# Kernel optimization log

Measured on AMD Instinct MI355X. Metric: run time of the kernel, lower is better.

The kernel has to match this reference:

```python
import jax, jax.numpy as jnp
import numpy as np

B, S, H, I, E, K = 2, 512, 1024, 4096, 8, 2
LN_EPS = 1e-5


def setup_inputs() -> dict:
    key = jax.random.key(0)
    ks = jax.random.split(key, 5)
    sc = 0.02  # init scale for weights
    return {
        "hidden_states": jax.random.normal(ks[0], (B, S, H), jnp.float32),
        "ln_w": jnp.ones((H,), jnp.float32),
        "ln_b": jnp.zeros((H,), jnp.float32),
        "Wr": jax.random.normal(ks[1], (E, H), jnp.float32) * sc,  # router [out=E, in=H]
        "br": jnp.zeros((E,), jnp.float32),
        "W1": jax.random.normal(ks[2], (E, I, H), jnp.float32) * sc,  # dense1 per expert [out=I, in=H]
        "b1": jnp.zeros((E, I), jnp.float32),
        "W2": jax.random.normal(ks[3], (E, H, I), jnp.float32) * sc,  # dense2 per expert [out=H, in=I]
        "b2": jnp.zeros((E, H), jnp.float32),
    }


def reference(hidden_states, ln_w, ln_b, Wr, br, W1, b1, W2, b2):
    # Eval mode: no jitter noise, no dropout.
    residual = hidden_states
    mu = jnp.mean(hidden_states, axis=-1, keepdims=True)
    var = jnp.mean(jnp.square(hidden_states - mu), axis=-1, keepdims=True)
    x = (hidden_states - mu) * jax.lax.rsqrt(var + LN_EPS) * ln_w + ln_b  # [B,S,H]

    logits = jnp.einsum("bsh,eh->bse", x, Wr) + br  # [B,S,E]
    topw, topi = jax.lax.top_k(logits, K)  # [B,S,K]
    topw = jax.nn.softmax(topw, axis=-1)
    # Combine weights per expert (top-k indices are distinct, so scatter == first-match)
    combine = jnp.sum(jax.nn.one_hot(topi, E, dtype=x.dtype) * topw[..., None], axis=-2)  # [B,S,E]

    # Dense per-expert FFN (reference form of gather-FFN-scatter); combine zeros out unselected experts
    a = jax.nn.gelu(jnp.einsum("bsh,eih->bsei", x, W1) + b1, approximate=False)  # [B,S,E,I]
    y = jnp.einsum("bsei,ehi->bseh", a, W2) + b2  # [B,S,E,H]
    out = residual + jnp.einsum("bse,bseh->bsh", combine, y)

    probs = jax.nn.softmax(logits, axis=-1)
    usage = jnp.mean(probs, axis=(0, 1))  # [E]
    balance_loss = E * jnp.sum(usage * usage) - 1.0
    return out, balance_loss
```

## Files before the change

### kernel.cpp

```cpp
#include <hip/hip_runtime.h>
#include <hip/hip_bf16.h>
#include <math.h>
#include <stdint.h>

#define T_TOK 1024
#define H_DIM 1024
#define I_DIM 4096
#define E_NUM 8
#define NSLOT (2 * T_TOK)

typedef __attribute__((ext_vector_type(8))) short bf16x8;
typedef __attribute__((ext_vector_type(4))) float f32x4;

#define MFMA_BF16(a, b, c) __builtin_amdgcn_mfma_f32_16x16x32_bf16(a, b, c, 0, 0, 0)

__device__ __forceinline__ short f2bf(float f) {
  union { float f; unsigned u; } x; x.f = f;
  unsigned r = (x.u + 0x7fffu + ((x.u >> 16) & 1u)) >> 16;
  return (short)r;
}
__device__ __forceinline__ int pack2bf(float a, float b) {
  return ((int)(unsigned short)f2bf(a)) | (((int)f2bf(b)) << 16);
}

typedef __attribute__((address_space(3))) unsigned int as3_u32;
typedef const __attribute__((address_space(1))) unsigned int as1_u32c;
__device__ __forceinline__ void glds16(const void* g, void* l) {
  __builtin_amdgcn_global_load_lds((as1_u32c*)g, (as3_u32*)l, 16, 0, 0);
}

__global__ __launch_bounds__(256) void k_ln_router(
    const float* __restrict__ x, const float* __restrict__ ln_w,
    const float* __restrict__ ln_b, const float* __restrict__ Wr,
    const float* __restrict__ br,
    short* __restrict__ xln, int* __restrict__ sel_e, float* __restrict__ sel_w,
    float* __restrict__ probs) {
  const int t = blockIdx.x;
  const int tid = threadIdx.x;
  const int lane = tid & 63, wid = tid >> 6;
  __shared__ float sx[H_DIM];
  __shared__ float redS[8];
  __shared__ float slog[E_NUM];

  float4 v = ((const float4*)(x + (size_t)t * H_DIM))[tid];
  float s = v.x + v.y + v.z + v.w;
  float ss = v.x * v.x + v.y * v.y + v.z * v.z + v.w * v.w;
  for (int o = 32; o > 0; o >>= 1) { s += __shfl_down(s, o); ss += __shfl_down(ss, o); }
  if (lane == 0) { redS[wid] = s; redS[4 + wid] = ss; }
  __syncthreads();
  float st = redS[0] + redS[1] + redS[2] + redS[3];
  float sst = redS[4] + redS[5] + redS[6] + redS[7];
  float mu = st * (1.0f / H_DIM);
  float var = sst * (1.0f / H_DIM) - mu * mu;
  float rs = rsqrtf(var + 1e-5f);

  float4 lw = ((const float4*)ln_w)[tid];
  float4 lb = ((const float4*)ln_b)[tid];
  float4 xn;
  xn.x = (v.x - mu) * rs * lw.x + lb.x;
  xn.y = (v.y - mu) * rs * lw.y + lb.y;
  xn.z = (v.z - mu) * rs * lw.z + lb.z;
  xn.w = (v.w - mu) * rs * lw.w + lb.w;
  sx[4 * tid + 0] = xn.x; sx[4 * tid + 1] = xn.y;
  sx[4 * tid + 2] = xn.z; sx[4 * tid + 3] = xn.w;
  short4 s4;
  s4.x = f2bf(xn.x); s4.y = f2bf(xn.y); s4.z = f2bf(xn.z); s4.w = f2bf(xn.w);
  ((short4*)(xln + (size_t)t * H_DIM))[tid] = s4;
  __syncthreads();

  for (int e = 2 * wid; e < 2 * wid + 2; ++e) {
    float p = 0.f;
    for (int h = lane; h < H_DIM; h += 64) p += sx[h] * Wr[e * H_DIM + h];
    for (int o = 32; o > 0; o >>= 1) p += __shfl_down(p, o);
    if (lane == 0) slog[e] = p + br[e];
  }
  __syncthreads();

  if (tid == 0) {
    float lg[E_NUM];
    for (int e = 0; e < E_NUM; ++e) lg[e] = slog[e];
    int i0 = 0;
    for (int e = 1; e < E_NUM; ++e) if (lg[e] > lg[i0]) i0 = e;
    int i1 = (i0 == 0) ? 1 : 0;
    for (int e = 0; e < E_NUM; ++e) if (e != i0 && lg[e] > lg[i1]) i1 = e;
    float w1e = __expf(lg[i1] - lg[i0]);
    float den = 1.f + w1e;
    sel_e[2 * t] = i0; sel_w[2 * t] = 1.f / den;
    sel_e[2 * t + 1] = i1; sel_w[2 * t + 1] = w1e / den;
    float se = 0.f, pe[E_NUM];
    for (int e = 0; e < E_NUM; ++e) { pe[e] = __expf(lg[e] - lg[i0]); se += pe[e]; }
    float inv = 1.f / se;
    for (int e = 0; e < E_NUM; ++e) probs[t * E_NUM + e] = pe[e] * inv;
  }
}

__global__ __launch_bounds__(512) void k_route(
    const int* __restrict__ sel_e, const float* __restrict__ probs,
    int* __restrict__ counts, int* __restrict__ basep,
    int* __restrict__ tlist, int* __restrict__ sel_idx,
    float* __restrict__ loss_out) {
  const int wid = threadIdx.x >> 6;
  const int lane = threadIdx.x & 63;
  __shared__ int scnt[E_NUM];
  __shared__ float susage[E_NUM];

  int cnt = 0;
  for (int s0 = 0; s0 < NSLOT; s0 += 64) {
    int s = s0 + lane;
    bool m = (sel_e[s] == wid);
    unsigned long long mk = __ballot(m);
    int pre = __popcll(mk & ((1ULL << lane) - 1ULL));
    if (m) {
      int idx = cnt + pre;
      sel_idx[s] = idx;
      tlist[wid * T_TOK + idx] = s >> 1;
    }
    cnt += __popcll(mk);
  }
  if (lane == 0) scnt[wid] = cnt;

  float u = 0.f;
  for (int t = lane; t < T_TOK; t += 64) u += probs[t * E_NUM + wid];
  for (int o = 32; o > 0; o >>= 1) u += __shfl_down(u, o);
  if (lane == 0) susage[wid] = u * (1.0f / T_TOK);
  __syncthreads();

  if (threadIdx.x == 0) {
    int b = 0;
    for (int e = 0; e < E_NUM; ++e) { basep[e] = b; counts[e] = scnt[e]; b += scnt[e]; }
    float sq = 0.f;
    for (int e = 0; e < E_NUM; ++e) sq += susage[e] * susage[e];
    *loss_out = (float)E_NUM * sq - 1.0f;
  }
}

__global__ __launch_bounds__(256) void k_ffn1(
    const short* __restrict__ xln, const float* __restrict__ W1,
    const float* __restrict__ b1, const int* __restrict__ counts,
    const int* __restrict__ basep, const int* __restrict__ tlist,
    short* __restrict__ a_buf) {
  const int e = blockIdx.z;
  const int cnt = counts[e];
  const int m0 = blockIdx.y * 128;
  if (m0 >= cnt) return;
  const int n0 = blockIdx.x * 128;

  __shared__ __align__(16) short As[128 * 32];
  __shared__ __align__(16) short Bs[128][40];

  const int tid = threadIdx.x;
  const int lane = tid & 63;
  const int wid = tid >> 6;
  const int wr = wid >> 1, wc = wid & 1;
  const int fr = lane & 15, fq = lane >> 4;

  const int arow = tid >> 2;
  const int au = (tid & 3) * 8;
  int r0 = m0 + arow;       if (r0 >= cnt) r0 = cnt - 1;
  int r1 = m0 + 64 + arow;  if (r1 >= cnt) r1 = cnt - 1;
  const short* ag0 = xln + (size_t)tlist[e * T_TOK + r0] * H_DIM + au;
  const short* ag1 = xln + (size_t)tlist[e * T_TOK + r1] * H_DIM + au;
  short* al0 = As + (size_t)tid * 8;
  short* al1 = As + (size_t)(256 + tid) * 8;

  const int bcol = (tid & 7) * 4;
  const int brow = tid >> 3;
  const float* bg = W1 + ((size_t)e * I_DIM + n0 + brow) * H_DIM + bcol;
  float4 breg[4];

#define LOADB(kk)                                                        \
  {                                                                      \
    _Pragma("unroll") for (int i = 0; i < 4; ++i)                        \
        breg[i] = *(const float4*)(bg + (size_t)(i * 32) * H_DIM + (kk));\
  }
#define CVTW()                                                           \
  {                                                                      \
    _Pragma("unroll") for (int i = 0; i < 4; ++i) {                      \
      int2 p;                                                            \
      p.x = pack2bf(breg[i].x, breg[i].y);                               \
      p.y = pack2bf(breg[i].z, breg[i].w);                               \
      *(int2*)&Bs[brow + i * 32][bcol] = p;                              \
    }                                                                    \
  }
#define GLDS(kk)                                                         \
  { glds16(ag0 + (kk), al0); glds16(ag1 + (kk), al1); }

  f32x4 acc[4][4];
#pragma unroll
  for (int i = 0; i < 4; ++i)
#pragma unroll
    for (int j = 0; j < 4; ++j) acc[i][j] = (f32x4)0.f;

  LOADB(0);
  GLDS(0);
  CVTW();
  __syncthreads();

  for (int kt = 0; kt < H_DIM / 32; ++kt) {
    const int kn = (kt + 1) * 32;
    const bool last = (kt == H_DIM / 32 - 1);
    if (!last) LOADB(kn);
    bf16x8 af[4], bb[4];
#pragma unroll
    for (int mi = 0; mi < 4; ++mi)
      af[mi] = *(const bf16x8*)(As + (wr * 64 + mi * 16 + fr) * 32 + fq * 8);
#pragma unroll
    for (int ni = 0; ni < 4; ++ni)
      bb[ni] = *(const bf16x8*)&Bs[wc * 64 + ni * 16 + fr][fq * 8];
#pragma unroll
    for (int mi = 0; mi < 4; ++mi)
#pragma unroll
      for (int ni = 0; ni < 4; ++ni)
        acc[mi][ni] = MFMA_BF16(af[mi], bb[ni], acc[mi][ni]);
    __syncthreads();
    if (!last) {
      GLDS(kn);
      CVTW();
      __syncthreads();
    }
  }

  const int slot0 = basep[e] + m0;
  float b1v[4];
#pragma unroll
  for (int ni = 0; ni < 4; ++ni)
    b1v[ni] = b1[e * I_DIM + n0 + wc * 64 + ni * 16 + fr];
#pragma unroll
  for (int mi = 0; mi < 4; ++mi)
#pragma unroll
    for (int j = 0; j < 4; ++j) {
      int r = wr * 64 + mi * 16 + fq * 4 + j;
      if (m0 + r < cnt) {
        size_t rowoff = (size_t)(slot0 + r) * I_DIM;
#pragma unroll
        for (int ni = 0; ni < 4; ++ni) {
          int colg = n0 + wc * 64 + ni * 16 + fr;
          float vv = acc[mi][ni][j] + b1v[ni];
          float g = 0.5f * vv * (1.0f + erff(vv * 0.70710678118654752f));
          a_buf[rowoff + colg] = f2bf(g);
        }
      }
    }
#undef LOADB
#undef CVTW
#undef GLDS
}

__global__ __launch_bounds__(256) void k_ffn2(
    const short* __restrict__ a_buf, const float* __restrict__ W2,
    const int* __restrict__ counts, const int* __restrict__ basep,
    float* __restrict__ y_part, int lg) {
  const int z = blockIdx.z;
  const int e = z >> lg;
  const int kc = z & ((1 << lg) - 1);
  const int CH = I_DIM >> lg;
  const int cnt = counts[e];
  const int m0 = blockIdx.y * 128;
  if (m0 >= cnt) return;
  const int n0 = blockIdx.x * 128;

  __shared__ __align__(16) short As[128 * 32];
  __shared__ __align__(16) short Bs[128][40];

  const int tid = threadIdx.x;
  const int lane = tid & 63;
  const int wid = tid >> 6;
  const int wr = wid >> 1, wc = wid & 1;
  const int fr = lane & 15, fq = lane >> 4;

  const int arow = tid >> 2;
  const int au = (tid & 3) * 8;
  int r0 = m0 + arow;       if (r0 >= cnt) r0 = cnt - 1;
  int r1 = m0 + 64 + arow;  if (r1 >= cnt) r1 = cnt - 1;
  const int sb = basep[e];
  const short* ag0 = a_buf + (size_t)(sb + r0) * I_DIM + kc * CH + au;
  const short* ag1 = a_buf + (size_t)(sb + r1) * I_DIM + kc * CH + au;
  short* al0 = As + (size_t)tid * 8;
  short* al1 = As + (size_t)(256 + tid) * 8;

  const int bcol = (tid & 7) * 4;
  const int brow = tid >> 3;
  const float* bg = W2 + ((size_t)e * H_DIM + n0 + brow) * I_DIM + kc * CH + bcol;
  float4 breg[4];

#define LOADB(kk)                                                        \
  {                                                                      \
    _Pragma("unroll") for (int i = 0; i < 4; ++i)                        \
        breg[i] = *(const float4*)(bg + (size_t)(i * 32) * I_DIM + (kk));\
  }
#define CVTW()                                                           \
  {                                                                      \
    _Pragma("unroll") for (int i = 0; i < 4; ++i) {                      \
      int2 p;                                                            \
      p.x = pack2bf(breg[i].x, breg[i].y);                               \
      p.y = pack2bf(breg[i].z, breg[i].w);                               \
      *(int2*)&Bs[brow + i * 32][bcol] = p;                              \
    }                                                                    \
  }
#define GLDS(kk)                                                         \
  { glds16(ag0 + (kk), al0); glds16(ag1 + (kk), al1); }

  f32x4 acc[4][4];
#pragma unroll
  for (int i = 0; i < 4; ++i)
#pragma unroll
    for (int j = 0; j < 4; ++j) acc[i][j] = (f32x4)0.f;

  LOADB(0);
  GLDS(0);
  CVTW();
  __syncthreads();

  const int KT = CH / 32;
  for (int kt = 0; kt < KT; ++kt) {
    const int kn = (kt + 1) * 32;
    const bool last = (kt == KT - 1);
    if (!last) LOADB(kn);
    bf16x8 af[4], bb[4];
#pragma unroll
    for (int mi = 0; mi < 4; ++mi)
      af[mi] = *(const bf16x8*)(As + (wr * 64 + mi * 16 + fr) * 32 + fq * 8);
#pragma unroll
    for (int ni = 0; ni < 4; ++ni)
      bb[ni] = *(const bf16x8*)&Bs[wc * 64 + ni * 16 + fr][fq * 8];
#pragma unroll
    for (int mi = 0; mi < 4; ++mi)
#pragma unroll
      for (int ni = 0; ni < 4; ++ni)
        acc[mi][ni] = MFMA_BF16(af[mi], bb[ni], acc[mi][ni]);
    __syncthreads();
    if (!last) {
      GLDS(kn);
      CVTW();
      __syncthreads();
    }
  }

  const int slot0 = sb + m0;
  float* yp = y_part + (size_t)kc * ((size_t)NSLOT * H_DIM);
#pragma unroll
  for (int mi = 0; mi < 4; ++mi)
#pragma unroll
    for (int j = 0; j < 4; ++j) {
      int r = wr * 64 + mi * 16 + fq * 4 + j;
      if (m0 + r < cnt) {
        size_t rowoff = (size_t)(slot0 + r) * H_DIM;
#pragma unroll
        for (int ni = 0; ni < 4; ++ni) {
          int colg = n0 + wc * 64 + ni * 16 + fr;
          yp[rowoff + colg] = acc[mi][ni][j];
        }
      }
    }
#undef LOADB
#undef CVTW
#undef GLDS
}

__global__ __launch_bounds__(256) void k_combine(
    const float* __restrict__ hidden, const float* __restrict__ y_part,
    const float* __restrict__ b2, const int* __restrict__ basep,
    const int* __restrict__ sel_e, const int* __restrict__ sel_idx,
    const float* __restrict__ sel_w, float* __restrict__ out, int KS) {
  const int t = blockIdx.x;
  const int tid = threadIdx.x;
  int e0 = sel_e[2 * t], e1 = sel_e[2 * t + 1];
  int s0 = basep[e0] + sel_idx[2 * t];
  int s1 = basep[e1] + sel_idx[2 * t + 1];
  float w0 = sel_w[2 * t], w1 = sel_w[2 * t + 1];
  const size_t TY = (size_t)NSLOT * H_DIM;
  float4 y0 = make_float4(0.f, 0.f, 0.f, 0.f);
  float4 y1 = make_float4(0.f, 0.f, 0.f, 0.f);
  for (int kc = 0; kc < KS; ++kc) {
    float4 p0 = ((const float4*)(y_part + kc * TY + (size_t)s0 * H_DIM))[tid];
    float4 p1 = ((const float4*)(y_part + kc * TY + (size_t)s1 * H_DIM))[tid];
    y0.x += p0.x; y0.y += p0.y; y0.z += p0.z; y0.w += p0.w;
    y1.x += p1.x; y1.y += p1.y; y1.z += p1.z; y1.w += p1.w;
  }
  float4 be0 = ((const float4*)(b2 + (size_t)e0 * H_DIM))[tid];
  float4 be1 = ((const float4*)(b2 + (size_t)e1 * H_DIM))[tid];
  float4 r = ((const float4*)(hidden + (size_t)t * H_DIM))[tid];
  float4 o;
  o.x = r.x + w0 * (y0.x + be0.x) + w1 * (y1.x + be1.x);
  o.y = r.y + w0 * (y0.y + be0.y) + w1 * (y1.y + be1.y);
  o.z = r.z + w0 * (y0.z + be0.z) + w1 * (y1.z + be1.z);
  o.w = r.w + w0 * (y0.w + be0.w) + w1 * (y1.w + be1.w);
  ((float4*)(out + (size_t)t * H_DIM))[tid] = o;
}

extern "C" void kernel_launch(void* const* d_in, const int* in_sizes, int n_in,
                              void* d_out, int out_size, void* d_ws, size_t ws_size,
                              hipStream_t stream) {
  const float* hidden = (const float*)d_in[0];
  const float* ln_w = (const float*)d_in[1];
  const float* ln_b = (const float*)d_in[2];
  const float* Wr = (const float*)d_in[3];
  const float* br = (const float*)d_in[4];
  const float* W1 = (const float*)d_in[5];
  const float* b1 = (const float*)d_in[6];
  const float* W2 = (const float*)d_in[7];
  const float* b2 = (const float*)d_in[8];
  float* out = (float*)d_out;

  char* w = (char*)d_ws;
  int* counts = (int*)(w + 0);
  int* basep = (int*)(w + 256);
  float* probs = (float*)(w + 512);
  int* tlist = (int*)(w + 33280);
  int* sel_e = (int*)(w + 66048);
  int* sel_idx = (int*)(w + 74240);
  float* sel_w = (float*)(w + 82432);
  short* xln = (short*)(w + 98304);
  short* a_buf = (short*)(w + 98304 + 2097152);
  const size_t Y_OFF = 98304 + 2097152 + 16777216;
  float* y_part = (float*)(w + Y_OFF);
  const size_t Y_SZ = (size_t)NSLOT * H_DIM * 4;
  int lg = 2;
  while (lg > 0 && Y_OFF + (Y_SZ << lg) > ws_size) --lg;
  const int KS = 1 << lg;

  k_ln_router<<<T_TOK, 256, 0, stream>>>(hidden, ln_w, ln_b, Wr, br, xln,
                                         sel_e, sel_w, probs);
  k_route<<<1, 512, 0, stream>>>(sel_e, probs, counts, basep, tlist, sel_idx,
                                 out + (size_t)T_TOK * H_DIM);
  k_ffn1<<<dim3(I_DIM / 128, T_TOK / 128, E_NUM), 256, 0, stream>>>(
      xln, W1, b1, counts, basep, tlist, a_buf);
  k_ffn2<<<dim3(H_DIM / 128, T_TOK / 128, E_NUM << lg), 256, 0, stream>>>(
      a_buf, W2, counts, basep, y_part, lg);
  k_combine<<<T_TOK, 256, 0, stream>>>(hidden, y_part, b2, basep, sel_e, sel_idx,
                                       sel_w, out, KS);
}
```

Before: 200.2 us.

## Double-buffer LDS in expert GEMMs and shrink N tile to 64

```diff
diff --git a/kernel.cpp b/kernel.cpp
--- a/kernel.cpp
+++ b/kernel.cpp
@@ -143,88 +143,78 @@
   const int cnt = counts[e];
   const int m0 = blockIdx.y * 128;
   if (m0 >= cnt) return;
-  const int n0 = blockIdx.x * 128;
-
-  __shared__ __align__(16) short As[128 * 32];
-  __shared__ __align__(16) short Bs[128][40];
+  const int n0 = blockIdx.x * 64;
+
+  __shared__ __align__(16) short As[2][4096];
+  __shared__ __align__(16) short Bs[2][64][40];
 
   const int tid = threadIdx.x;
-  const int lane = tid & 63;
-  const int wid = tid >> 6;
+  const int lane = tid & 63, wid = tid >> 6;
   const int wr = wid >> 1, wc = wid & 1;
   const int fr = lane & 15, fq = lane >> 4;
 
-  const int arow = tid >> 2;
-  const int au = (tid & 3) * 8;
-  int r0 = m0 + arow;       if (r0 >= cnt) r0 = cnt - 1;
-  int r1 = m0 + 64 + arow;  if (r1 >= cnt) r1 = cnt - 1;
-  const short* ag0 = xln + (size_t)tlist[e * T_TOK + r0] * H_DIM + au;
-  const short* ag1 = xln + (size_t)tlist[e * T_TOK + r1] * H_DIM + au;
-  short* al0 = As + (size_t)tid * 8;
-  short* al1 = As + (size_t)(256 + tid) * 8;
-
-  const int bcol = (tid & 7) * 4;
-  const int brow = tid >> 3;
-  const float* bg = W1 + ((size_t)e * I_DIM + n0 + brow) * H_DIM + bcol;
-  float4 breg[4];
-
-#define LOADB(kk)                                                        \
-  {                                                                      \
-    _Pragma("unroll") for (int i = 0; i < 4; ++i)                        \
-        breg[i] = *(const float4*)(bg + (size_t)(i * 32) * H_DIM + (kk));\
-  }
-#define CVTW()                                                           \
-  {                                                                      \
-    _Pragma("unroll") for (int i = 0; i < 4; ++i) {                      \
-      int2 p;                                                            \
-      p.x = pack2bf(breg[i].x, breg[i].y);                               \
-      p.y = pack2bf(breg[i].z, breg[i].w);                               \
-      *(int2*)&Bs[brow + i * 32][bcol] = p;                              \
-    }                                                                    \
-  }
-#define GLDS(kk)                                                         \
-  { glds16(ag0 + (kk), al0); glds16(ag1 + (kk), al1); }
-
-  f32x4 acc[4][4];
-#pragma unroll
-  for (int i = 0; i < 4; ++i)
-#pragma unroll
-    for (int j = 0; j < 4; ++j) acc[i][j] = (f32x4)0.f;
-
-  LOADB(0);
-  GLDS(0);
-  CVTW();
-  __syncthreads();
-
+  const int arow = tid & 127;
+  const int afq = tid >> 7;
+  int rA = m0 + arow; if (rA >= cnt) rA = cnt - 1;
+  const short* ag = xln + (size_t)tlist[e * T_TOK + rA] * H_DIM + afq * 8;
+
+  const int brow = tid >> 2, bseg = (tid & 3) * 8;
+  const float* bg = W1 + ((size_t)e * I_DIM + n0 + brow) * H_DIM + bseg;
+
+  f32x4 acc[4][2];
+#pragma unroll
+  for (int i = 0; i < 4; ++i) { acc[i][0] = (f32x4)0.f; acc[i][1] = (f32x4)0.f; }
+
+  float4 b0 = *(const float4*)(bg);
+  float4 b1r = *(const float4*)(bg + 4);
+  glds16(ag, &As[0][(size_t)tid * 8]);
+  glds16(ag + 16, &As[0][(size_t)(256 + tid) * 8]);
+  {
+    int4 p;
+    p.x = pack2bf(b0.x, b0.y); p.y = pack2bf(b0.z, b0.w);
+    p.z = pack2bf(b1r.x, b1r.y); p.w = pack2bf(b1r.z, b1r.w);
+    *(int4*)&Bs[0][brow][bseg] = p;
+  }
+  __syncthreads();
+
+  int cur = 0;
   for (int kt = 0; kt < H_DIM / 32; ++kt) {
     const int kn = (kt + 1) * 32;
-    const bool last = (kt == H_DIM / 32 - 1);
-    if (!last) LOADB(kn);
-    bf16x8 af[4], bb[4];
+    const bool pf = (kt + 1 < H_DIM / 32);
+    float4 nb0, nb1;
+    if (pf) {
+      glds16(ag + kn, &As[cur ^ 1][(size_t)tid * 8]);
+      glds16(ag + kn + 16, &As[cur ^ 1][(size_t)(256 + tid) * 8]);
+      nb0 = *(const float4*)(bg + kn);
+      nb1 = *(const float4*)(bg + kn + 4);
+    }
+    bf16x8 af[4], bb[2];
 #pragma unroll
     for (int mi = 0; mi < 4; ++mi)
-      af[mi] = *(const bf16x8*)(As + (wr * 64 + mi * 16 + fr) * 32 + fq * 8);
-#pragma unroll
-    for (int ni = 0; ni < 4; ++ni)
-      bb[ni] = *(const bf16x8*)&Bs[wc * 64 + ni * 16 + fr][fq * 8];
+      af[mi] = *(const bf16x8*)&As[cur][(fq * 128 + wr * 64 + mi * 16 + fr) * 8];
+#pragma unroll
+    for (int ni = 0; ni < 2; ++ni)
+      bb[ni] = *(const bf16x8*)&Bs[cur][wc * 32 + ni * 16 + fr][fq * 8];
 #pragma unroll
     for (int mi = 0; mi < 4; ++mi)
 #pragma unroll
-      for (int ni = 0; ni < 4; ++ni)
+      for (int ni = 0; ni < 2; ++ni)
         acc[mi][ni] = MFMA_BF16(af[mi], bb[ni], acc[mi][ni]);
+    if (pf) {
+      int4 p;
+      p.x = pack2bf(nb0.x, nb0.y); p.y = pack2bf(nb0.z, nb0.w);
+      p.z = pack2bf(nb1.x, nb1.y); p.w = pack2bf(nb1.z, nb1.w);
+      *(int4*)&Bs[cur ^ 1][brow][bseg] = p;
+    }
     __syncthreads();
-    if (!last) {
-      GLDS(kn);
-      CVTW();
-      __syncthreads();
-    }
+    cur ^= 1;
   }
 
   const int slot0 = basep[e] + m0;
-  float b1v[4];
-#pragma unroll
-  for (int ni = 0; ni < 4; ++ni)
-    b1v[ni] = b1[e * I_DIM + n0 + wc * 64 + ni * 16 + fr];
+  float b1v[2];
+#pragma unroll
+  for (int ni = 0; ni < 2; ++ni)
+    b1v[ni] = b1[e * I_DIM + n0 + wc * 32 + ni * 16 + fr];
 #pragma unroll
   for (int mi = 0; mi < 4; ++mi)
 #pragma unroll
@@ -233,17 +223,14 @@
       if (m0 + r < cnt) {
         size_t rowoff = (size_t)(slot0 + r) * I_DIM;
 #pragma unroll
-        for (int ni = 0; ni < 4; ++ni) {
-          int colg = n0 + wc * 64 + ni * 16 + fr;
+        for (int ni = 0; ni < 2; ++ni) {
+          int colg = n0 + wc * 32 + ni * 16 + fr;
           float vv = acc[mi][ni][j] + b1v[ni];
           float g = 0.5f * vv * (1.0f + erff(vv * 0.70710678118654752f));
           a_buf[rowoff + colg] = f2bf(g);
         }
       }
     }
-#undef LOADB
-#undef CVTW
-#undef GLDS
 }
 
 __global__ __launch_bounds__(256) void k_ffn2(
@@ -257,83 +244,73 @@
   const int cnt = counts[e];
   const int m0 = blockIdx.y * 128;
   if (m0 >= cnt) return;
-  const int n0 = blockIdx.x * 128;
-
-  __shared__ __align__(16) short As[128 * 32];
-  __shared__ __align__(16) short Bs[128][40];
+  const int n0 = blockIdx.x * 64;
+
+  __shared__ __align__(16) short As[2][4096];
+  __shared__ __align__(16) short Bs[2][64][40];
 
   const int tid = threadIdx.x;
-  const int lane = tid & 63;
-  const int wid = tid >> 6;
+  const int lane = tid & 63, wid = tid >> 6;
   const int wr = wid >> 1, wc = wid & 1;
   const int fr = lane & 15, fq = lane >> 4;
 
-  const int arow = tid >> 2;
-  const int au = (tid & 3) * 8;
-  int r0 = m0 + arow;       if (r0 >= cnt) r0 = cnt - 1;
-  int r1 = m0 + 64 + arow;  if (r1 >= cnt) r1 = cnt - 1;
+  const int arow = tid & 127;
+  const int afq = tid >> 7;
+  int rA = m0 + arow; if (rA >= cnt) rA = cnt - 1;
   const int sb = basep[e];
-  const short* ag0 = a_buf + (size_t)(sb + r0) * I_DIM + kc * CH + au;
-  const short* ag1 = a_buf + (size_t)(sb + r1) * I_DIM + kc * CH + au;
-  short* al0 = As + (size_t)tid * 8;
-  short* al1 = As + (size_t)(256 + tid) * 8;
-
-  const int bcol = (tid & 7) * 4;
-  const int brow = tid >> 3;
-  const float* bg = W2 + ((size_t)e * H_DIM + n0 + brow) * I_DIM + kc * CH + bcol;
-  float4 breg[4];
-
-#define LOADB(kk)                                                        \
-  {                                                                      \
-    _Pragma("unroll") for (int i = 0; i < 4; ++i)                        \
-        breg[i] = *(const float4*)(bg + (size_t)(i * 32) * I_DIM + (kk));\
-  }
-#define CVTW()                                                           \
-  {                                                                      \
-    _Pragma("unroll") for (int i = 0; i < 4; ++i) {                      \
-      int2 p;                                                            \
-      p.x = pack2bf(breg[i].x, breg[i].y);                               \
-      p.y = pack2bf(breg[i].z, breg[i].w);                               \
-      *(int2*)&Bs[brow + i * 32][bcol] = p;                              \
-    }                                                                    \
-  }
-#define GLDS(kk)                                                         \
-  { glds16(ag0 + (kk), al0); glds16(ag1 + (kk), al1); }
-
-  f32x4 acc[4][4];
-#pragma unroll
-  for (int i = 0; i < 4; ++i)
-#pragma unroll
-    for (int j = 0; j < 4; ++j) acc[i][j] = (f32x4)0.f;
-
-  LOADB(0);
-  GLDS(0);
-  CVTW();
+  const short* ag = a_buf + (size_t)(sb + rA) * I_DIM + kc * CH + afq * 8;
+
+  const int brow = tid >> 2, bseg = (tid & 3) * 8;
+  const float* bg = W2 + ((size_t)e * H_DIM + n0 + brow) * I_DIM + kc * CH + bseg;
+
+  f32x4 acc[4][2];
+#pragma unroll
+  for (int i = 0; i < 4; ++i) { acc[i][0] = (f32x4)0.f; acc[i][1] = (f32x4)0.f; }
+
+  float4 b0 = *(const float4*)(bg);
+  float4 b1r = *(const float4*)(bg + 4);
+  glds16(ag, &As[0][(size_t)tid * 8]);
+  glds16(ag + 16, &As[0][(size_t)(256 + tid) * 8]);
+  {
+    int4 p;
+    p.x = pack2bf(b0.x, b0.y); p.y = pack2bf(b0.z, b0.w);
+    p.z = pack2bf(b1r.x, b1r.y); p.w = pack2bf(b1r.z, b1r.w);
+    *(int4*)&Bs[0][brow][bseg] = p;
+  }
   __syncthreads();
 
   const int KT = CH / 32;
+  int cur = 0;
   for (int kt = 0; kt < KT; ++kt) {
     const int kn = (kt + 1) * 32;
-    const bool last = (kt == KT - 1);
-    if (!last) LOADB(kn);
-    bf16x8 af[4], bb[4];
+    const bool pf = (kt + 1 < KT);
+    float4 nb0, nb1;
+    if (pf) {
+      glds16(ag + kn, &As[cur ^ 1][(size_t)tid * 8]);
+      glds16(ag + kn + 16, &As[cur ^ 1][(size_t)(256 + tid) * 8]);
+      nb0 = *(const float4*)(bg + kn);
+      nb1 = *(const float4*)(bg + kn + 4);
+    }
+    bf16x8 af[4], bb[2];
 #pragma unroll
     for (int mi = 0; mi < 4; ++mi)
-      af[mi] = *(const bf16x8*)(As + (wr * 64 + mi * 16 + fr) * 32 + fq * 8);
-#pragma unroll
-    for (int ni = 0; ni < 4; ++ni)
-      bb[ni] = *(const bf16x8*)&Bs[wc * 64 + ni * 16 + fr][fq * 8];
+      af[mi] = *(const bf16x8*)&As[cur][(fq * 128 + wr * 64 + mi * 16 + fr) * 8];
+#pragma unroll
+    for (int ni = 0; ni < 2; ++ni)
+      bb[ni] = *(const bf16x8*)&Bs[cur][wc * 32 + ni * 16 + fr][fq * 8];
 #pragma unroll
     for (int mi = 0; mi < 4; ++mi)
 #pragma unroll
-      for (int ni = 0; ni < 4; ++ni)
+      for (int ni = 0; ni < 2; ++ni)
         acc[mi][ni] = MFMA_BF16(af[mi], bb[ni], acc[mi][ni]);
+    if (pf) {
+      int4 p;
+      p.x = pack2bf(nb0.x, nb0.y); p.y = pack2bf(nb0.z, nb0.w);
+      p.z = pack2bf(nb1.x, nb1.y); p.w = pack2bf(nb1.z, nb1.w);
+      *(int4*)&Bs[cur ^ 1][brow][bseg] = p;
+    }
     __syncthreads();
-    if (!last) {
-      GLDS(kn);
-      CVTW();
-      __syncthreads();
-    }
+    cur ^= 1;
   }
 
   const int slot0 = sb + m0;
@@ -346,15 +323,12 @@
       if (m0 + r < cnt) {
         size_t rowoff = (size_t)(slot0 + r) * H_DIM;
 #pragma unroll
-        for (int ni = 0; ni < 4; ++ni) {
-          int colg = n0 + wc * 64 + ni * 16 + fr;
+        for (int ni = 0; ni < 2; ++ni) {
+          int colg = n0 + wc * 32 + ni * 16 + fr;
           yp[rowoff + colg] = acc[mi][ni][j];
         }
       }
     }
-#undef LOADB
-#undef CVTW
-#undef GLDS
 }
 
 __global__ __launch_bounds__(256) void k_combine(
@@ -423,9 +397,9 @@
                                          sel_e, sel_w, probs);
   k_route<<<1, 512, 0, stream>>>(sel_e, probs, counts, basep, tlist, sel_idx,
                                  out + (size_t)T_TOK * H_DIM);
-  k_ffn1<<<dim3(I_DIM / 128, T_TOK / 128, E_NUM), 256, 0, stream>>>(
+  k_ffn1<<<dim3(I_DIM / 64, T_TOK / 128, E_NUM), 256, 0, stream>>>(
       xln, W1, b1, counts, basep, tlist, a_buf);
-  k_ffn2<<<dim3(H_DIM / 128, T_TOK / 128, E_NUM << lg), 256, 0, stream>>>(
+  k_ffn2<<<dim3(H_DIM / 64, T_TOK / 128, E_NUM << lg), 256, 0, stream>>>(
       a_buf, W2, counts, basep, y_part, lg);
   k_combine<<<T_TOK, 256, 0, stream>>>(hidden, y_part, b2, basep, sel_e, sel_idx,
                                        sel_w, out, KS);
```

Result: slower. 254.2 us (+27.0%).

## Double-buffer FFN GEMMs with direct fp32 weight loads to swizzled LDS

Applied to the files above, without the earlier changes.

```diff
diff --git a/kernel.cpp b/kernel.cpp
--- a/kernel.cpp
+++ b/kernel.cpp
@@ -28,6 +28,8 @@
 __device__ __forceinline__ void glds16(const void* g, void* l) {
   __builtin_amdgcn_global_load_lds((as1_u32c*)g, (as3_u32*)l, 16, 0, 0);
 }
+
+union BBCast { int4 i4; bf16x8 v; };
 
 __global__ __launch_bounds__(256) void k_ln_router(
     const float* __restrict__ x, const float* __restrict__ ln_w,
@@ -145,45 +147,22 @@
   if (m0 >= cnt) return;
   const int n0 = blockIdx.x * 128;
 
-  __shared__ __align__(16) short As[128 * 32];
-  __shared__ __align__(16) short Bs[128][40];
+  __shared__ __align__(16) short As[2][128 * 32];
+  __shared__ __align__(16) float Bsf[2][128 * 32];
 
   const int tid = threadIdx.x;
-  const int lane = tid & 63;
-  const int wid = tid >> 6;
+  const int lane = tid & 63, wid = tid >> 6;
   const int wr = wid >> 1, wc = wid & 1;
   const int fr = lane & 15, fq = lane >> 4;
 
-  const int arow = tid >> 2;
-  const int au = (tid & 3) * 8;
-  int r0 = m0 + arow;       if (r0 >= cnt) r0 = cnt - 1;
-  int r1 = m0 + 64 + arow;  if (r1 >= cnt) r1 = cnt - 1;
-  const short* ag0 = xln + (size_t)tlist[e * T_TOK + r0] * H_DIM + au;
-  const short* ag1 = xln + (size_t)tlist[e * T_TOK + r1] * H_DIM + au;
-  short* al0 = As + (size_t)tid * 8;
-  short* al1 = As + (size_t)(256 + tid) * 8;
-
-  const int bcol = (tid & 7) * 4;
-  const int brow = tid >> 3;
-  const float* bg = W1 + ((size_t)e * I_DIM + n0 + brow) * H_DIM + bcol;
-  float4 breg[4];
-
-#define LOADB(kk)                                                        \
-  {                                                                      \
-    _Pragma("unroll") for (int i = 0; i < 4; ++i)                        \
-        breg[i] = *(const float4*)(bg + (size_t)(i * 32) * H_DIM + (kk));\
-  }
-#define CVTW()                                                           \
-  {                                                                      \
-    _Pragma("unroll") for (int i = 0; i < 4; ++i) {                      \
-      int2 p;                                                            \
-      p.x = pack2bf(breg[i].x, breg[i].y);                               \
-      p.y = pack2bf(breg[i].z, breg[i].w);                               \
-      *(int2*)&Bs[brow + i * 32][bcol] = p;                              \
-    }                                                                    \
-  }
-#define GLDS(kk)                                                         \
-  { glds16(ag0 + (kk), al0); glds16(ag1 + (kk), al1); }
+  int r0 = m0 + (tid >> 2); if (r0 >= cnt) r0 = cnt - 1;
+  int r1 = m0 + 64 + (tid >> 2); if (r1 >= cnt) r1 = cnt - 1;
+  const short* ag0 = xln + (size_t)tlist[e * T_TOK + r0] * H_DIM + (tid & 3) * 8;
+  const short* ag1 = xln + (size_t)tlist[e * T_TOK + r1] * H_DIM + (tid & 3) * 8;
+
+  const int bro = tid >> 3;
+  const int bslot = (tid & 7) ^ (bro & 7);
+  const float* bg = W1 + ((size_t)e * I_DIM + n0 + bro) * H_DIM + bslot * 4;
 
   f32x4 acc[4][4];
 #pragma unroll
@@ -191,33 +170,44 @@
 #pragma unroll
     for (int j = 0; j < 4; ++j) acc[i][j] = (f32x4)0.f;
 
-  LOADB(0);
-  GLDS(0);
-  CVTW();
-  __syncthreads();
-
+#define STAGE(kk, buf)                                                      \
+  {                                                                         \
+    glds16(ag0 + (kk), &As[buf][tid * 8]);                                  \
+    glds16(ag1 + (kk), &As[buf][(256 + tid) * 8]);                          \
+    _Pragma("unroll") for (int i = 0; i < 4; ++i)                           \
+        glds16(bg + (size_t)(i * 32) * H_DIM + (kk),                        \
+               &Bsf[buf][(i * 256 + tid) * 4]);                             \
+  }
+
+  STAGE(0, 0);
+  __syncthreads();
+
+  int cur = 0;
   for (int kt = 0; kt < H_DIM / 32; ++kt) {
-    const int kn = (kt + 1) * 32;
-    const bool last = (kt == H_DIM / 32 - 1);
-    if (!last) LOADB(kn);
+    if (kt + 1 < H_DIM / 32) STAGE((kt + 1) * 32, cur ^ 1);
     bf16x8 af[4], bb[4];
 #pragma unroll
     for (int mi = 0; mi < 4; ++mi)
-      af[mi] = *(const bf16x8*)(As + (wr * 64 + mi * 16 + fr) * 32 + fq * 8);
-#pragma unroll
-    for (int ni = 0; ni < 4; ++ni)
-      bb[ni] = *(const bf16x8*)&Bs[wc * 64 + ni * 16 + fr][fq * 8];
+      af[mi] = *(const bf16x8*)&As[cur][(wr * 64 + mi * 16 + fr) * 32 + fq * 8];
+#pragma unroll
+    for (int ni = 0; ni < 4; ++ni) {
+      const int row = wc * 64 + ni * 16 + fr;
+      const int base = row * 128 + fq * 32;
+      const int sw = (row & 7) << 4;
+      f32x4 lo = *(const f32x4*)((const char*)&Bsf[cur][0] + (base ^ sw));
+      f32x4 hi = *(const f32x4*)((const char*)&Bsf[cur][0] + ((base + 16) ^ sw));
+      BBCast c;
+      c.i4.x = pack2bf(lo[0], lo[1]); c.i4.y = pack2bf(lo[2], lo[3]);
+      c.i4.z = pack2bf(hi[0], hi[1]); c.i4.w = pack2bf(hi[2], hi[3]);
+      bb[ni] = c.v;
+    }
 #pragma unroll
     for (int mi = 0; mi < 4; ++mi)
 #pragma unroll
       for (int ni = 0; ni < 4; ++ni)
         acc[mi][ni] = MFMA_BF16(af[mi], bb[ni], acc[mi][ni]);
     __syncthreads();
-    if (!last) {
-      GLDS(kn);
-      CVTW();
-      __syncthreads();
-    }
+    cur ^= 1;
   }
 
   const int slot0 = basep[e] + m0;
@@ -241,9 +231,7 @@
         }
       }
     }
-#undef LOADB
-#undef CVTW
-#undef GLDS
+#undef STAGE
 }
 
 __global__ __launch_bounds__(256) void k_ffn2(
@@ -259,46 +247,23 @@
   if (m0 >= cnt) return;
   const int n0 = blockIdx.x * 128;
 
-  __shared__ __align__(16) short As[128 * 32];
-  __shared__ __align__(16) short Bs[128][40];
+  __shared__ __align__(16) short As[2][128 * 32];
+  __shared__ __align__(16) float Bsf[2][128 * 32];
 
   const int tid = threadIdx.x;
-  const int lane = tid & 63;
-  const int wid = tid >> 6;
+  const int lane = tid & 63, wid = tid >> 6;
   const int wr = wid >> 1, wc = wid & 1;
   const int fr = lane & 15, fq = lane >> 4;
 
-  const int arow = tid >> 2;
-  const int au = (tid & 3) * 8;
-  int r0 = m0 + arow;       if (r0 >= cnt) r0 = cnt - 1;
-  int r1 = m0 + 64 + arow;  if (r1 >= cnt) r1 = cnt - 1;
+  int r0 = m0 + (tid >> 2); if (r0 >= cnt) r0 = cnt - 1;
+  int r1 = m0 + 64 + (tid >> 2); if (r1 >= cnt) r1 = cnt - 1;
   const int sb = basep[e];
-  const short* ag0 = a_buf + (size_t)(sb + r0) * I_DIM + kc * CH + au;
-  const short* ag1 = a_buf + (size_t)(sb + r1) * I_DIM + kc * CH + au;
-  short* al0 = As + (size_t)tid * 8;
-  short* al1 = As + (size_t)(256 + tid) * 8;
-
-  const int bcol = (tid & 7) * 4;
-  const int brow = tid >> 3;
-  const float* bg = W2 + ((size_t)e * H_DIM + n0 + brow) * I_DIM + kc * CH + bcol;
-  float4 breg[4];
-
-#define LOADB(kk)                                                        \
-  {                                                                      \
-    _Pragma("unroll") for (int i = 0; i < 4; ++i)                        \
-        breg[i] = *(const float4*)(bg + (size_t)(i * 32) * I_DIM + (kk));\
-  }
-#define CVTW()                                                           \
-  {                                                                      \
-    _Pragma("unroll") for (int i = 0; i < 4; ++i) {                      \
-      int2 p;                                                            \
-      p.x = pack2bf(breg[i].x, breg[i].y);                               \
-      p.y = pack2bf(breg[i].z, breg[i].w);                               \
-      *(int2*)&Bs[brow + i * 32][bcol] = p;                              \
-    }                                                                    \
-  }
-#define GLDS(kk)                                                         \
-  { glds16(ag0 + (kk), al0); glds16(ag1 + (kk), al1); }
+  const short* ag0 = a_buf + (size_t)(sb + r0) * I_DIM + kc * CH + (tid & 3) * 8;
+  const short* ag1 = a_buf + (size_t)(sb + r1) * I_DIM + kc * CH + (tid & 3) * 8;
+
+  const int bro = tid >> 3;
+  const int bslot = (tid & 7) ^ (bro & 7);
+  const float* bg = W2 + ((size_t)e * H_DIM + n0 + bro) * I_DIM + kc * CH + bslot * 4;
 
   f32x4 acc[4][4];
 #pragma unroll
@@ -306,34 +271,45 @@
 #pragma unroll
     for (int j = 0; j < 4; ++j) acc[i][j] = (f32x4)0.f;
 
-  LOADB(0);
-  GLDS(0);
-  CVTW();
+#define STAGE(kk, buf)                                                      \
+  {                                                                         \
+    glds16(ag0 + (kk), &As[buf][tid * 8]);                                  \
+    glds16(ag1 + (kk), &As[buf][(256 + tid) * 8]);                          \
+    _Pragma("unroll") for (int i = 0; i < 4; ++i)                           \
+        glds16(bg + (size_t)(i * 32) * I_DIM + (kk),                        \
+               &Bsf[buf][(i * 256 + tid) * 4]);                             \
+  }
+
+  STAGE(0, 0);
   __syncthreads();
 
   const int KT = CH / 32;
+  int cur = 0;
   for (int kt = 0; kt < KT; ++kt) {
-    const int kn = (kt + 1) * 32;
-    const bool last = (kt == KT - 1);
-    if (!last) LOADB(kn);
+    if (kt + 1 < KT) STAGE((kt + 1) * 32, cur ^ 1);
     bf16x8 af[4], bb[4];
 #pragma unroll
     for (int mi = 0; mi < 4; ++mi)
-      af[mi] = *(const bf16x8*)(As + (wr * 64 + mi * 16 + fr) * 32 + fq * 8);
-#pragma unroll
-    for (int ni = 0; ni < 4; ++ni)
-      bb[ni] = *(const bf16x8*)&Bs[wc * 64 + ni * 16 + fr][fq * 8];
+      af[mi] = *(const bf16x8*)&As[cur][(wr * 64 + mi * 16 + fr) * 32 + fq * 8];
+#pragma unroll
+    for (int ni = 0; ni < 4; ++ni) {
+      const int row = wc * 64 + ni * 16 + fr;
+      const int base = row * 128 + fq * 32;
+      const int sw = (row & 7) << 4;
+      f32x4 lo = *(const f32x4*)((const char*)&Bsf[cur][0] + (base ^ sw));
+      f32x4 hi = *(const f32x4*)((const char*)&Bsf[cur][0] + ((base + 16) ^ sw));
+      BBCast c;
+      c.i4.x = pack2bf(lo[0], lo[1]); c.i4.y = pack2bf(lo[2], lo[3]);
+      c.i4.z = pack2bf(hi[0], hi[1]); c.i4.w = pack2bf(hi[2], hi[3]);
+      bb[ni] = c.v;
+    }
 #pragma unroll
     for (int mi = 0; mi < 4; ++mi)
 #pragma unroll
       for (int ni = 0; ni < 4; ++ni)
         acc[mi][ni] = MFMA_BF16(af[mi], bb[ni], acc[mi][ni]);
     __syncthreads();
-    if (!last) {
-      GLDS(kn);
-      CVTW();
-      __syncthreads();
-    }
+    cur ^= 1;
   }
 
   const int slot0 = sb + m0;
@@ -352,9 +328,7 @@
         }
       }
     }
-#undef LOADB
-#undef CVTW
-#undef GLDS
+#undef STAGE
 }
 
 __global__ __launch_bounds__(256) void k_combine(
@@ -415,7 +389,7 @@
   const size_t Y_OFF = 98304 + 2097152 + 16777216;
   float* y_part = (float*)(w + Y_OFF);
   const size_t Y_SZ = (size_t)NSLOT * H_DIM * 4;
-  int lg = 2;
+  int lg = 3;
   while (lg > 0 && Y_OFF + (Y_SZ << lg) > ws_size) --lg;
   const int KS = 1 << lg;
 
```

Result: slower. 267.2 us (+33.5%).
